# Optimization experiments

Hardware: AMD Instinct MI355X
Metric: run time of the kernel (lower is better)

Reference implementation:

```python
import jax, jax.numpy as jnp
import numpy as np

N_ROOMS = 128
N = 2 + N_ROOMS          # 2 external wall nodes + room nodes
T = 131072               # number of evaluation times
DT = 30.0                # seconds between evaluations
Q_LIM = 500.0
K_SCALE = 1e-5           # physical scaling of sigmoid(params) -> conductances [1/s]
DAY = 86400.0
TOUT_N = 1100            # hourly outside-temperature table covering the horizon


def setup_inputs() -> dict:
    key = jax.random.key(0)
    k1, k2, k3, k4 = jax.random.split(key, 4)
    t_eval = jnp.arange(T, dtype=jnp.float32) * DT
    params = jax.random.uniform(k1, (N * N,), dtype=jnp.float32)      # torch.rand init
    heating = jax.random.normal(k2, (N_ROOMS, 3), dtype=jnp.float32)  # torch.randn init
    B = jnp.zeros((N, 1 + N_ROOMS), dtype=jnp.float32)
    B = B.at[:, 0].set(jax.random.uniform(k3, (N,), dtype=jnp.float32) * 1e-5)  # Tout coupling
    B = B.at[2:, 1:].set(jnp.eye(N_ROOMS, dtype=jnp.float32) * 1e-6)           # heat input per room
    tout_t = jnp.arange(TOUT_N, dtype=jnp.float32) * 3600.0
    tout_v = 10.0 + 5.0 * jax.random.normal(k4, (TOUT_N,), dtype=jnp.float32)
    return {"t_eval": t_eval, "params": params, "heating": heating, "B": B,
            "tout_t": tout_t, "tout_v": tout_v}


def _forward(t_eval, params, heating, B, tout_t, tout_v):
    # transform + physical scaling of parameters -> RC conductance matrix A
    theta = jax.nn.sigmoid(params) * K_SCALE
    K = theta.reshape(N, N)
    d = jnp.diag(K)
    Koff = K - jnp.diag(d)
    A = Koff - jnp.diag(Koff.sum(axis=1) + d)   # Metzler, nonpositive row sums -> stable

    # transform + heat scaling -> continuous heating profile Qrms_continuous
    Q_avg = jax.nn.sigmoid(heating[:, 0]) * Q_LIM
    phase = heating[:, 1]
    sharp = heating[:, 2]

    t0 = t_eval[0]
    te = t_eval - t0
    two_pi = 2.0 * jnp.pi

    def Tout(t):  # Tout_continuous (linear interp, like scipy interp1d)
        return jnp.interp(t + t0, tout_t, tout_v)

    def Qf(t):    # smooth periodic heating schedule per room
        return Q_avg * jax.nn.sigmoid(sharp * jnp.sin(two_pi * (t + t0) / DAY + phase))

    def f(t, x):  # dx/dt = A @ x + B @ u
        u = jnp.concatenate([Tout(t)[None], Qf(t)])[:, None]   # [1+R, 1]
        return A @ x + B @ u

    iv = (Tout(te[0]) + 4.0) * jnp.ones((N, 1), dtype=jnp.float32)

    def step(x, tt):  # one RK4 step between consecutive evaluation times
        t, dt = tt
        half = dt * 0.5
        k1 = f(t, x)
        k2 = f(t + half, x + half * k1)
        k3 = f(t + half, x + half * k2)
        k4 = f(t + dt, x + dt * k3)
        xn = x + (dt / 6.0) * (k1 + 2.0 * k2 + 2.0 * k3 + k4)
        return xn, xn

    ts = te[:-1]
    dts = te[1:] - te[:-1]
    _, xs = jax.lax.scan(step, iv, (ts, dts))
    sol = jnp.concatenate([iv[None], xs], axis=0)   # [T, N, 1]
    return sol[:, 2:]                               # room temperatures only


def reference(t_eval, params, heating, B, tout_t, tout_v):
    return _forward(t_eval, params, heating, B, tout_t, tout_v)
```

## Files before the change

### kernel.cpp

```cpp
#include <hip/hip_runtime.h>
#include <math.h>

#define NPAD 132
#define TSTEPS 131071
#define LCH 128
#define NCH 1024
#define PERIOD 2880
#define OMEGA 7.2722052166430399e-05f

#define OFF_A    0
#define OFF_A2   17160
#define OFF_A3   34320
#define OFF_M    51480
#define OFF_C1   68640
#define OFF_C2   85800
#define OFF_P1   102960
#define OFF_P2   120120
#define OFF_M64  137280
#define OFF_M128 154440
#define OFF_M2K  171600
#define OFF_C1T  188760
#define OFF_C2T  205144
#define OFF_C1B  221528
#define OFF_C2B  221658
#define OFF_C3B  221788
#define OFF_AMP  221918
#define OFF_CPH  222046
#define OFF_SPH  222174
#define OFF_SH   222302
#define OFF_G    222430
#define OFF_S64  355550
#define OFF_XB   488670
#define OFF_XB2  621790
#define OFF_SA   888030
#define OFF_GP   896350
#define OFF_TT   1270750

__device__ __forceinline__ float sigm(float x) { return 1.0f / (1.0f + expf(-x)); }

__device__ __forceinline__ float interp_tout(float t, const float* __restrict__ tv) {
    float u = t * (1.0f / 3600.0f);
    int idx = (int)u;
    if (idx > 1098) idx = 1098;
    float fr = u - (float)idx;
    float v0 = tv[idx];
    return v0 + fr * (tv[idx + 1] - v0);
}

__global__ __launch_bounds__(256) void build_A_kernel(
    const float* __restrict__ params, const float* __restrict__ heating,
    const float* __restrict__ Bm, const float* __restrict__ tout_v,
    float* __restrict__ ws, float* __restrict__ out) {
    const int tid = threadIdx.x;
    float* A = ws + OFF_A;

    for (int idx = tid; idx < 130 * 130; idx += 256) {
        int r = idx / 130, c = idx - r * 130;
        A[r * NPAD + c] = sigm(params[idx]) * 1e-5f;
    }
    for (int r = tid; r < 130; r += 256) { A[r * NPAD + 130] = 0.f; A[r * NPAD + 131] = 0.f; }
    __syncthreads();
    for (int r = tid; r < 130; r += 256) {
        float s = 0.0f;
        for (int k = 0; k < 130; ++k) s += A[r * NPAD + k];
        A[r * NPAD + r] = -s;
    }
    for (int i = tid; i < 128; i += 256) {
        float bd = Bm[(2 + i) * 129 + (1 + i)];
        ws[OFF_AMP + i] = sigm(heating[i * 3]) * 500.0f * bd;
        float ph = heating[i * 3 + 1];
        ws[OFF_CPH + i] = cosf(ph);
        ws[OFF_SPH + i] = sinf(ph);
        ws[OFF_SH + i]  = heating[i * 3 + 2];
    }
    float iv = tout_v[0] + 4.0f;
    for (int i = tid; i < 128; i += 256) out[i] = iv;
    for (int r = tid; r < 130; r += 256) ws[OFF_XB + r] = iv;
}

__global__ __launch_bounds__(192) void mm_kernel(float* __restrict__ ws,
                                                 int offD, int offX, int offY) {
    const float* X = ws + offX;
    const float* Y = ws + offY;
    float* dst = ws + offD;
    __shared__ float xrow[130];
    const int r = blockIdx.x;
    const int c = threadIdx.x;
    if (c < 130) xrow[c] = X[r * NPAD + c];
    __syncthreads();
    if (c < 130) {
        float acc = 0.0f;
#pragma unroll 10
        for (int k = 0; k < 130; ++k)
            acc = fmaf(xrow[k], Y[k * NPAD + c], acc);
        dst[r * NPAD + c] = acc;
    }
    if (c >= 130 && c < 132) dst[r * NPAD + c] = 0.0f;
}

__global__ __launch_bounds__(192) void mm34_kernel(float* __restrict__ ws) {
    const int b = blockIdx.x;
    const bool hi = (b >= 130);
    const int r = hi ? b - 130 : b;
    const float* X = ws + (hi ? OFF_A2 : OFF_A);
    const float* Y = ws + OFF_A2;
    float* dst = ws + (hi ? OFF_P2 : OFF_A3);
    __shared__ float xrow[130];
    const int c = threadIdx.x;
    if (c < 130) xrow[c] = X[r * NPAD + c];
    __syncthreads();
    if (c < 130) {
        float acc = 0.0f;
#pragma unroll 10
        for (int k = 0; k < 130; ++k)
            acc = fmaf(xrow[k], Y[k * NPAD + c], acc);
        dst[r * NPAD + c] = acc;
    }
    if (c >= 130 && c < 132) dst[r * NPAD + c] = 0.0f;
}

__global__ __launch_bounds__(256) void combine_kernel(float* __restrict__ ws) {
    int idx = blockIdx.x * 256 + threadIdx.x;
    if (idx >= 130 * 130) return;
    int r = idx / 130, c = idx - r * 130;
    int o = r * NPAD + c;
    const float* A  = ws + OFF_A;
    const float* A2 = ws + OFF_A2;
    const float* A3 = ws + OFF_A3;
    const float* A4 = ws + OFF_P2;
    float eye = (r == c) ? 1.0f : 0.0f;
    float a = A[o], a2 = A2[o], a3 = A3[o], a4 = A4[o];
    float c1v = 5.0f * eye + 150.0f * a + 2250.0f * a2 + 33750.0f * a3;
    float c2v = 20.0f * eye + 300.0f * a + 2250.0f * a2;
    ws[OFF_M  + o] = eye + 30.0f * a + 450.0f * a2 + 4500.0f * a3 + 33750.0f * a4;
    ws[OFF_C1 + o] = c1v;
    ws[OFF_C2 + o] = c2v;
    if (r >= 2 && c >= 2) {
        ws[OFF_C1T + (c - 2) * 128 + (r - 2)] = c1v;
        ws[OFF_C2T + (c - 2) * 128 + (r - 2)] = c2v;
    }
    if (c == 0) {
        ws[OFF_M + r * NPAD + 130] = 0.f; ws[OFF_M + r * NPAD + 131] = 0.f;
        ws[OFF_C1 + r * NPAD + 130] = 0.f; ws[OFF_C1 + r * NPAD + 131] = 0.f;
        ws[OFF_C2 + r * NPAD + 130] = 0.f; ws[OFF_C2 + r * NPAD + 131] = 0.f;
    }
}

__global__ __launch_bounds__(192) void vecs_kernel(const float* __restrict__ Bm,
                                                   float* __restrict__ ws) {
    const int r = threadIdx.x;
    if (r >= 130) return;
    const float* C1 = ws + OFF_C1;
    const float* C2 = ws + OFF_C2;
    float s1 = 0.0f, s2 = 0.0f;
    for (int k = 0; k < 130; ++k) {
        float b0 = Bm[k * 129];
        s1 = fmaf(C1[r * NPAD + k], b0, s1);
        s2 = fmaf(C2[r * NPAD + k], b0, s2);
    }
    ws[OFF_C1B + r] = s1;
    ws[OFF_C2B + r] = s2;
    ws[OFF_C3B + r] = 5.0f * Bm[r * 129];
}

__global__ __launch_bounds__(256) void gper_kernel(float* __restrict__ ws) {
    const int tid = threadIdx.x;
    const int n0 = blockIdx.x * 32;
    const float* C1T = ws + OFF_C1T;
    const float* C2T = ws + OFF_C2T;
    const float* C1 = ws + OFF_C1;
    const float* C2 = ws + OFF_C2;
    const float* amp = ws + OFF_AMP;
    const float* cph = ws + OFF_CPH;
    const float* sph = ws + OFF_SPH;
    const float* sh  = ws + OFF_SH;
    float* P = ws + OFF_GP;

    __shared__ __align__(16) float qgT[128][36];
    __shared__ __align__(16) float qmT[128][36];
    __shared__ float sth[65], cth[65];

    for (int j = tid; j < 65; j += 256) {
        float t = (j < 33) ? (float)(n0 + j) * 30.0f
                           : (float)(n0 + j - 33) * 30.0f + 15.0f;
        float a = t * OMEGA;
        sth[j] = sinf(a);
        cth[j] = cosf(a);
    }
    __syncthreads();

    for (int p = tid; p < 65 * 128; p += 256) {
        int j = p >> 7, i = p & 127;
        float s = sth[j] * cph[i] + cth[j] * sph[i];
        float v = amp[i] / (1.0f + __expf(-sh[i] * s));
        if (j < 33) qgT[i][j] = v; else qmT[i][j - 33] = v;
    }
    __syncthreads();

    const int rr = tid & 127;
    const int half = tid >> 7;
    const int r = rr + 2;
    float acc1[16], acc2[16];
#pragma unroll
    for (int w = 0; w < 16; ++w) { acc1[w] = 0.0f; acc2[w] = 0.0f; }

    for (int k = 0; k < 128; ++k) {
        float c1 = C1T[(k << 7) + rr];
        float c2 = C2T[(k << 7) + rr];
        const float4* q1p = reinterpret_cast<const float4*>(&qgT[k][half * 16]);
        const float4* q2p = reinterpret_cast<const float4*>(&qmT[k][half * 16]);
#pragma unroll
        for (int w = 0; w < 4; ++w) {
            float4 a = q1p[w];
            float4 b = q2p[w];
            acc1[4 * w + 0] = fmaf(c1, a.x, acc1[4 * w + 0]);
            acc1[4 * w + 1] = fmaf(c1, a.y, acc1[4 * w + 1]);
            acc1[4 * w + 2] = fmaf(c1, a.z, acc1[4 * w + 2]);
            acc1[4 * w + 3] = fmaf(c1, a.w, acc1[4 * w + 3]);
            acc2[4 * w + 0] = fmaf(c2, b.x, acc2[4 * w + 0]);
            acc2[4 * w + 1] = fmaf(c2, b.y, acc2[4 * w + 1]);
            acc2[4 * w + 2] = fmaf(c2, b.z, acc2[4 * w + 2]);
            acc2[4 * w + 3] = fmaf(c2, b.w, acc2[4 * w + 3]);
        }
    }
#pragma unroll
    for (int w = 0; w < 16; ++w) {
        int n = half * 16 + w;
        P[(n0 + n) * 130 + r] = acc1[w] + acc2[w] + 5.0f * qgT[rr][n + 1];
    }

    if (tid < 64) {
        int r2 = tid >> 5;
        int n = tid & 31;
        float acc = 0.0f;
        for (int k = 0; k < 128; ++k) {
            acc = fmaf(C1[r2 * NPAD + 2 + k], qgT[k][n], acc);
            acc = fmaf(C2[r2 * NPAD + 2 + k], qmT[k][n], acc);
        }
        P[(n0 + n) * 130 + r2] = acc;
    }
}

__global__ __launch_bounds__(256) void ttab_kernel(const float* __restrict__ tout_v,
                                                   float* __restrict__ ws) {
    int n = blockIdx.x * 256 + threadIdx.x;
    if (n < 131072) {
        float t = (float)n * 30.0f;
        float2* TT = reinterpret_cast<float2*>(ws + OFF_TT);
        TT[n] = make_float2(interp_tout(t, tout_v), interp_tout(t + 15.0f, tout_v));
    }
}

__global__ __launch_bounds__(192, 3) void chunk_accum_kernel(float* __restrict__ ws) {
    const int c = blockIdx.x;
    const int r = threadIdx.x;
    const float* Mm = ws + OFF_M;
    const float* P = ws + OFF_GP;
    const float2* TT = reinterpret_cast<const float2*>(ws + OFF_TT);

    __shared__ __align__(16) float xs[2][132];
    float4 mr[33];
    float c1br = 0.f, c2br = 0.f, c3br = 0.f;
    if (r < 130) {
#pragma unroll
        for (int q = 0; q < 33; ++q)
            mr[q] = reinterpret_cast<const float4*>(&Mm[r * NPAD])[q];
        c1br = ws[OFF_C1B + r]; c2br = ws[OFF_C2B + r]; c3br = ws[OFF_C3B + r];
    }
    if (r < 132) { xs[0][r] = 0.0f; xs[1][r] = 0.0f; }
    __syncthreads();

    const int base = c * LCH;
    const int len = min(LCH, TSTEPS - base);
    int m = base % PERIOD;
    float pv = (r < 130) ? P[m * 130 + r] : 0.0f;
    float2 tc = TT[base], tn = TT[base + 1];
    int cur = 0;
    for (int j = 0; j < len; ++j) {
        if (r < 130) {
            float gcur = pv + tc.x * c1br + tc.y * c2br + tn.x * c3br;
            m = (m + 1 == PERIOD) ? 0 : m + 1;
            if (j + 1 < len) { pv = P[m * 130 + r]; tc = tn; tn = TT[base + j + 2]; }
            const float4* xp = reinterpret_cast<const float4*>(xs[cur]);
            float a0 = 0.f, a1 = 0.f, a2 = 0.f, a3 = 0.f;
#pragma unroll
            for (int q = 0; q < 33; ++q) {
                float4 xv = xp[q];
                a0 = fmaf(mr[q].x, xv.x, a0);
                a1 = fmaf(mr[q].y, xv.y, a1);
                a2 = fmaf(mr[q].z, xv.z, a2);
                a3 = fmaf(mr[q].w, xv.w, a3);
            }
            float val = (a0 + a1) + (a2 + a3) + gcur;
            xs[cur ^ 1][r] = val;
            if (j == 63) ws[OFF_S64 + c * 130 + r] = val;
        }
        __syncthreads();
        cur ^= 1;
    }
    if (r < 130) ws[OFF_G + c * 130 + r] = xs[cur][r];
}

__global__ __launch_bounds__(192, 3) void superaccum_kernel(float* __restrict__ ws) {
    const int s = blockIdx.x;
    const int r = threadIdx.x;
    const float* MP = ws + OFF_M128;
    const float* G = ws + OFF_G;

    __shared__ __align__(16) float xs[2][132];
    float4 mr[33];
    if (r < 130) {
#pragma unroll
        for (int q = 0; q < 33; ++q)
            mr[q] = reinterpret_cast<const float4*>(&MP[r * NPAD])[q];
    }
    if (r < 132) { xs[0][r] = 0.0f; xs[1][r] = 0.0f; }
    __syncthreads();

    int cur = 0;
    for (int i = 0; i < 16; ++i) {
        if (r < 130) {
            const float4* xp = reinterpret_cast<const float4*>(xs[cur]);
            float a0 = 0.f, a1 = 0.f, a2 = 0.f, a3 = 0.f;
#pragma unroll
            for (int q = 0; q < 33; ++q) {
                float4 xv = xp[q];
                a0 = fmaf(mr[q].x, xv.x, a0);
                a1 = fmaf(mr[q].y, xv.y, a1);
                a2 = fmaf(mr[q].z, xv.z, a2);
                a3 = fmaf(mr[q].w, xv.w, a3);
            }
            xs[cur ^ 1][r] = (a0 + a1) + (a2 + a3) + G[(16 * s + i) * 130 + r];
        }
        __syncthreads();
        cur ^= 1;
    }
    if (r < 130) ws[OFF_SA + s * 130 + r] = xs[cur][r];
}

__global__ __launch_bounds__(192, 3) void superbound_kernel(float* __restrict__ ws) {
    const int r = threadIdx.x;
    const float* M2K = ws + OFF_M2K;
    const float* SA = ws + OFF_SA;
    float* xb = ws + OFF_XB;

    __shared__ __align__(16) float xs[2][132];
    float4 mr[33];
    if (r < 130) {
#pragma unroll
        for (int q = 0; q < 33; ++q)
            mr[q] = reinterpret_cast<const float4*>(&M2K[r * NPAD])[q];
    }
    if (r < 132) { xs[0][r] = (r < 130) ? xb[r] : 0.0f; xs[1][r] = 0.0f; }
    __syncthreads();

    int cur = 0;
    for (int s = 0; s < 63; ++s) {
        if (r < 130) {
            const float4* xp = reinterpret_cast<const float4*>(xs[cur]);
            float a0 = 0.f, a1 = 0.f, a2 = 0.f, a3 = 0.f;
#pragma unroll
            for (int q = 0; q < 33; ++q) {
                float4 xv = xp[q];
                a0 = fmaf(mr[q].x, xv.x, a0);
                a1 = fmaf(mr[q].y, xv.y, a1);
                a2 = fmaf(mr[q].z, xv.z, a2);
                a3 = fmaf(mr[q].w, xv.w, a3);
            }
            float val = (a0 + a1) + (a2 + a3) + SA[s * 130 + r];
            xs[cur ^ 1][r] = val;
            xb[(16 * s + 16) * 130 + r] = val;
        }
        __syncthreads();
        cur ^= 1;
    }
}

__global__ __launch_bounds__(192, 3) void chunkbound_kernel(float* __restrict__ ws) {
    const int s = blockIdx.x;
    const int r = threadIdx.x;
    const float* MP = ws + OFF_M128;
    const float* G = ws + OFF_G;
    float* xb = ws + OFF_XB;

    __shared__ __align__(16) float xs[2][132];
    float4 mr[33];
    if (r < 130) {
#pragma unroll
        for (int q = 0; q < 33; ++q)
            mr[q] = reinterpret_cast<const float4*>(&MP[r * NPAD])[q];
    }
    if (r < 132) { xs[0][r] = (r < 130) ? xb[(16 * s) * 130 + r] : 0.0f; xs[1][r] = 0.0f; }
    __syncthreads();

    int cur = 0;
    for (int i = 0; i < 15; ++i) {
        if (r < 130) {
            const float4* xp = reinterpret_cast<const float4*>(xs[cur]);
            float a0 = 0.f, a1 = 0.f, a2 = 0.f, a3 = 0.f;
#pragma unroll
            for (int q = 0; q < 33; ++q) {
                float4 xv = xp[q];
                a0 = fmaf(mr[q].x, xv.x, a0);
                a1 = fmaf(mr[q].y, xv.y, a1);
                a2 = fmaf(mr[q].z, xv.z, a2);
                a3 = fmaf(mr[q].w, xv.w, a3);
            }
            float val = (a0 + a1) + (a2 + a3) + G[(16 * s + i) * 130 + r];
            xs[cur ^ 1][r] = val;
            xb[(16 * s + i + 1) * 130 + r] = val;
        }
        __syncthreads();
        cur ^= 1;
    }
}

__global__ __launch_bounds__(192, 3) void subbound_kernel(float* __restrict__ ws) {
    const int c = blockIdx.x;
    const int r = threadIdx.x;
    const float* M64 = ws + OFF_M64;
    const float* xb = ws + OFF_XB;
    float* xb2 = ws + OFF_XB2;

    __shared__ __align__(16) float xs[132];
    if (r < 132) xs[r] = (r < 130) ? xb[c * 130 + r] : 0.0f;
    __syncthreads();
    if (r < 130) {
        const float4* xp = reinterpret_cast<const float4*>(xs);
        const float4* mp = reinterpret_cast<const float4*>(&M64[r * NPAD]);
        float a0 = 0.f, a1 = 0.f, a2 = 0.f, a3 = 0.f;
#pragma unroll
        for (int q = 0; q < 33; ++q) {
            float4 m = mp[q];
            float4 xv = xp[q];
            a0 = fmaf(m.x, xv.x, a0);
            a1 = fmaf(m.y, xv.y, a1);
            a2 = fmaf(m.z, xv.z, a2);
            a3 = fmaf(m.w, xv.w, a3);
        }
        xb2[(2 * c) * 130 + r] = xs[r];
        xb2[(2 * c + 1) * 130 + r] = (a0 + a1) + (a2 + a3) + ws[OFF_S64 + c * 130 + r];
    }
}

__global__ __launch_bounds__(192, 3) void chunk_emit_kernel(float* __restrict__ ws,
                                                            float* __restrict__ out) {
    const int ec = blockIdx.x;
    const int r = threadIdx.x;
    const float* Mm = ws + OFF_M;
    const float* P = ws + OFF_GP;
    const float2* TT = reinterpret_cast<const float2*>(ws + OFF_TT);
    const float* xb2 = ws + OFF_XB2;

    __shared__ __align__(16) float xs[2][132];
    float4 mr[33];
    float c1br = 0.f, c2br = 0.f, c3br = 0.f;
    if (r < 130) {
#pragma unroll
        for (int q = 0; q < 33; ++q)
            mr[q] = reinterpret_cast<const float4*>(&Mm[r * NPAD])[q];
        c1br = ws[OFF_C1B + r]; c2br = ws[OFF_C2B + r]; c3br = ws[OFF_C3B + r];
    }
    if (r < 132) { xs[0][r] = (r < 130) ? xb2[ec * 130 + r] : 0.0f; xs[1][r] = 0.0f; }
    __syncthreads();

    const int base = ec * 64;
    const int len = min(64, TSTEPS - base);
    int m = base % PERIOD;
    float pv = (r < 130) ? P[m * 130 + r] : 0.0f;
    float2 tc = TT[base], tn = TT[base + 1];
    int cur = 0;
    for (int j = 0; j < len; ++j) {
        if (r < 130) {
            float gcur = pv + tc.x * c1br + tc.y * c2br + tn.x * c3br;
            m = (m + 1 == PERIOD) ? 0 : m + 1;
            if (j + 1 < len) { pv = P[m * 130 + r]; tc = tn; tn = TT[base + j + 2]; }
            const float4* xp = reinterpret_cast<const float4*>(xs[cur]);
            float a0 = 0.f, a1 = 0.f, a2 = 0.f, a3 = 0.f;
#pragma unroll
            for (int q = 0; q < 33; ++q) {
                float4 xv = xp[q];
                a0 = fmaf(mr[q].x, xv.x, a0);
                a1 = fmaf(mr[q].y, xv.y, a1);
                a2 = fmaf(mr[q].z, xv.z, a2);
                a3 = fmaf(mr[q].w, xv.w, a3);
            }
            float val = (a0 + a1) + (a2 + a3) + gcur;
            xs[cur ^ 1][r] = val;
            if (r >= 2) out[(base + j + 1) * 128 + (r - 2)] = val;
        }
        __syncthreads();
        cur ^= 1;
    }
}

extern "C" void kernel_launch(void* const* d_in, const int* in_sizes, int n_in,
                              void* d_out, int out_size, void* d_ws, size_t ws_size,
                              hipStream_t stream) {
    const float* params  = (const float*)d_in[1];
    const float* heating = (const float*)d_in[2];
    const float* Bm      = (const float*)d_in[3];
    const float* tout_v  = (const float*)d_in[5];
    float* out = (float*)d_out;
    float* ws = (float*)d_ws;

    build_A_kernel<<<1, 256, 0, stream>>>(params, heating, Bm, tout_v, ws, out);

    mm_kernel<<<130, 192, 0, stream>>>(ws, OFF_A2, OFF_A, OFF_A);
    mm34_kernel<<<260, 192, 0, stream>>>(ws);
    combine_kernel<<<67, 256, 0, stream>>>(ws);
    vecs_kernel<<<1, 192, 0, stream>>>(Bm, ws);
    gper_kernel<<<90, 256, 0, stream>>>(ws);
    ttab_kernel<<<512, 256, 0, stream>>>(tout_v, ws);

    mm_kernel<<<130, 192, 0, stream>>>(ws, OFF_P1,   OFF_M,    OFF_M);
    mm_kernel<<<130, 192, 0, stream>>>(ws, OFF_P2,   OFF_P1,   OFF_P1);
    mm_kernel<<<130, 192, 0, stream>>>(ws, OFF_P1,   OFF_P2,   OFF_P2);
    mm_kernel<<<130, 192, 0, stream>>>(ws, OFF_P2,   OFF_P1,   OFF_P1);
    mm_kernel<<<130, 192, 0, stream>>>(ws, OFF_P1,   OFF_P2,   OFF_P2);
    mm_kernel<<<130, 192, 0, stream>>>(ws, OFF_M64,  OFF_P1,   OFF_P1);
    mm_kernel<<<130, 192, 0, stream>>>(ws, OFF_M128, OFF_M64,  OFF_M64);
    mm_kernel<<<130, 192, 0, stream>>>(ws, OFF_P1,   OFF_M128, OFF_M128);
    mm_kernel<<<130, 192, 0, stream>>>(ws, OFF_P2,   OFF_P1,   OFF_P1);
    mm_kernel<<<130, 192, 0, stream>>>(ws, OFF_P1,   OFF_P2,   OFF_P2);
    mm_kernel<<<130, 192, 0, stream>>>(ws, OFF_M2K,  OFF_P1,   OFF_P1);

    chunk_accum_kernel<<<NCH, 192, 0, stream>>>(ws);
    superaccum_kernel<<<63, 192, 0, stream>>>(ws);
    superbound_kernel<<<1, 192, 0, stream>>>(ws);
    chunkbound_kernel<<<64, 192, 0, stream>>>(ws);
    subbound_kernel<<<NCH, 192, 0, stream>>>(ws);
    chunk_emit_kernel<<<2 * NCH, 192, 0, stream>>>(ws, out);
}
```

Measured before the change: 537.1 us.

## Stride-4 chunk accumulation using M^4 and precomputed 4-step forcing tables

The chunk accumulation pass now advances four RK4 steps per matrix-vector product using M^4. It uses a doubled periodic forcing table (GP4, built by two new pdouble kernels) and nine per-row weights for the outside-temperature samples, precomputed in vecs2. This cuts the serial matvec-and-barrier count in the accumulation phase by a factor of four, at the cost of extra setup kernels and more workspace. Launch bounds drop from 3 to 2 blocks per CU, and inline asm pins keep the matrix rows in registers. This may reduce occupancy and changes rounding order.

```diff
diff --git a/kernel.cpp b/kernel.cpp
--- a/kernel.cpp
+++ b/kernel.cpp
@@ -16,25 +16,32 @@
 #define OFF_C2   85800
 #define OFF_P1   102960
 #define OFF_P2   120120
-#define OFF_M64  137280
-#define OFF_M128 154440
-#define OFF_M2K  171600
-#define OFF_C1T  188760
-#define OFF_C2T  205144
-#define OFF_C1B  221528
-#define OFF_C2B  221658
-#define OFF_C3B  221788
-#define OFF_AMP  221918
-#define OFF_CPH  222046
-#define OFF_SPH  222174
-#define OFF_SH   222302
-#define OFF_G    222430
-#define OFF_S64  355550
-#define OFF_XB   488670
-#define OFF_XB2  621790
-#define OFF_SA   888030
-#define OFF_GP   896350
-#define OFF_TT   1270750
+#define OFF_M2   137280
+#define OFF_M4   154440
+#define OFF_M64  171600
+#define OFF_M128 188760
+#define OFF_M2K  205920
+#define OFF_C1T  223080
+#define OFF_C2T  239464
+#define OFF_C1B  255848
+#define OFF_C2B  255978
+#define OFF_C3B  256108
+#define OFF_AMP  256238
+#define OFF_CPH  256366
+#define OFF_SPH  256494
+#define OFF_SH   256622
+#define OFF_W    256750
+#define OFF_G    257920
+#define OFF_S64  391040
+#define OFF_XB   524160
+#define OFF_XB2  657280
+#define OFF_SA   923520
+#define OFF_GP   931710
+#define OFF_GP2  1306110
+#define OFF_GP4  1680510
+#define OFF_TT   2054910
+
+#define PIN4(v) asm volatile("" : "+v"((v).x), "+v"((v).y), "+v"((v).z), "+v"((v).w))
 
 __device__ __forceinline__ float sigm(float x) { return 1.0f / (1.0f + expf(-x)); }
 
@@ -146,21 +153,59 @@
     }
 }
 
-__global__ __launch_bounds__(192) void vecs_kernel(const float* __restrict__ Bm,
-                                                   float* __restrict__ ws) {
+__global__ __launch_bounds__(192) void vecs2_kernel(const float* __restrict__ Bm,
+                                                    float* __restrict__ ws) {
     const int r = threadIdx.x;
-    if (r >= 130) return;
     const float* C1 = ws + OFF_C1;
     const float* C2 = ws + OFF_C2;
-    float s1 = 0.0f, s2 = 0.0f;
-    for (int k = 0; k < 130; ++k) {
-        float b0 = Bm[k * 129];
-        s1 = fmaf(C1[r * NPAD + k], b0, s1);
-        s2 = fmaf(C2[r * NPAD + k], b0, s2);
-    }
-    ws[OFF_C1B + r] = s1;
-    ws[OFF_C2B + r] = s2;
-    ws[OFF_C3B + r] = 5.0f * Bm[r * 129];
+    const float* Mm = ws + OFF_M;
+    __shared__ __align__(16) float va[132], vb[132], vd[132];
+    __shared__ __align__(16) float na[132], nb[132], nd[132];
+    __shared__ float a1s[130], a2s[130], c1bs[130];
+
+    if (r < 132) { va[r] = 0.f; vb[r] = 0.f; vd[r] = 0.f; na[r] = 0.f; nb[r] = 0.f; nd[r] = 0.f; }
+    __syncthreads();
+    if (r < 130) {
+        float s1 = 0.0f, s2 = 0.0f;
+        for (int k = 0; k < 130; ++k) {
+            float b0 = Bm[k * 129];
+            s1 = fmaf(C1[r * NPAD + k], b0, s1);
+            s2 = fmaf(C2[r * NPAD + k], b0, s2);
+        }
+        float c3 = 5.0f * Bm[r * 129];
+        ws[OFF_C1B + r] = s1; ws[OFF_C2B + r] = s2; ws[OFF_C3B + r] = c3;
+        ws[OFF_W + 7 * 130 + r] = s2;
+        ws[OFF_W + 8 * 130 + r] = c3;
+        va[r] = s1; vb[r] = s2; vd[r] = c3; c1bs[r] = s1;
+    }
+    __syncthreads();
+
+    for (int st = 1; st <= 3; ++st) {
+        if (r < 130) {
+            const float4* mp = reinterpret_cast<const float4*>(&Mm[r * NPAD]);
+            const float4* pa = reinterpret_cast<const float4*>(va);
+            const float4* pb = reinterpret_cast<const float4*>(vb);
+            const float4* pd = reinterpret_cast<const float4*>(vd);
+            float aa = 0.f, ab = 0.f, ad = 0.f;
+#pragma unroll
+            for (int q = 0; q < 33; ++q) {
+                float4 m = mp[q];
+                float4 xa = pa[q], xb = pb[q], xd = pd[q];
+                aa = fmaf(m.x, xa.x, fmaf(m.y, xa.y, fmaf(m.z, xa.z, fmaf(m.w, xa.w, aa))));
+                ab = fmaf(m.x, xb.x, fmaf(m.y, xb.y, fmaf(m.z, xb.z, fmaf(m.w, xb.w, ab))));
+                ad = fmaf(m.x, xd.x, fmaf(m.y, xd.y, fmaf(m.z, xd.z, fmaf(m.w, xd.w, ad))));
+            }
+            na[r] = aa; nb[r] = ab; nd[r] = ad;
+        }
+        __syncthreads();
+        if (r < 130) {
+            if (st == 1) { ws[OFF_W + 5 * 130 + r] = nb[r]; ws[OFF_W + 6 * 130 + r] = nd[r] + c1bs[r]; a1s[r] = na[r]; }
+            if (st == 2) { ws[OFF_W + 3 * 130 + r] = nb[r]; ws[OFF_W + 4 * 130 + r] = nd[r] + a1s[r]; a2s[r] = na[r]; }
+            if (st == 3) { ws[OFF_W + 0 * 130 + r] = na[r]; ws[OFF_W + 1 * 130 + r] = nb[r]; ws[OFF_W + 2 * 130 + r] = nd[r] + a2s[r]; }
+            va[r] = na[r]; vb[r] = nb[r]; vd[r] = nd[r];
+        }
+        __syncthreads();
+    }
 }
 
 __global__ __launch_bounds__(256) void gper_kernel(float* __restrict__ ws) {
@@ -241,46 +286,88 @@
     }
 }
 
+__global__ __launch_bounds__(192) void pdouble_kernel(float* __restrict__ ws,
+                                                      int offD, int offS, int offMat, int shift) {
+    const int m0 = blockIdx.x * 16;
+    const int tid = threadIdx.x;
+    const float* S = ws + offS;
+    const float* Mat = ws + offMat;
+    float* D = ws + offD;
+    __shared__ __align__(16) float xs2[16][132];
+    for (int p = tid; p < 16 * 132; p += 192) {
+        int i = p / 132, rr = p - i * 132;
+        xs2[i][rr] = (rr < 130) ? S[(m0 + i) * 130 + rr] : 0.0f;
+    }
+    __syncthreads();
+    const int r = tid;
+    if (r < 130) {
+        float acc[16];
+#pragma unroll
+        for (int i = 0; i < 16; ++i) acc[i] = 0.0f;
+        const float4* mp = reinterpret_cast<const float4*>(&Mat[r * NPAD]);
+        for (int q = 0; q < 33; ++q) {
+            float4 m = mp[q];
+#pragma unroll
+            for (int i = 0; i < 16; ++i) {
+                float4 x = reinterpret_cast<const float4*>(xs2[i])[q];
+                acc[i] = fmaf(m.x, x.x, fmaf(m.y, x.y, fmaf(m.z, x.z, fmaf(m.w, x.w, acc[i]))));
+            }
+        }
+#pragma unroll
+        for (int i = 0; i < 16; ++i) {
+            int ms = m0 + i + shift; if (ms >= PERIOD) ms -= PERIOD;
+            D[(m0 + i) * 130 + r] = acc[i] + S[ms * 130 + r];
+        }
+    }
+}
+
 __global__ __launch_bounds__(256) void ttab_kernel(const float* __restrict__ tout_v,
                                                    float* __restrict__ ws) {
     int n = blockIdx.x * 256 + threadIdx.x;
-    if (n < 131072) {
+    if (n < 131080) {
         float t = (float)n * 30.0f;
         float2* TT = reinterpret_cast<float2*>(ws + OFF_TT);
         TT[n] = make_float2(interp_tout(t, tout_v), interp_tout(t + 15.0f, tout_v));
     }
 }
 
-__global__ __launch_bounds__(192, 3) void chunk_accum_kernel(float* __restrict__ ws) {
+__global__ __launch_bounds__(192, 2) void chunk_accum_kernel(float* __restrict__ ws) {
     const int c = blockIdx.x;
     const int r = threadIdx.x;
-    const float* Mm = ws + OFF_M;
-    const float* P = ws + OFF_GP;
+    const float* M4 = ws + OFF_M4;
+    const float* P4 = ws + OFF_GP4;
     const float2* TT = reinterpret_cast<const float2*>(ws + OFF_TT);
 
     __shared__ __align__(16) float xs[2][132];
     float4 mr[33];
-    float c1br = 0.f, c2br = 0.f, c3br = 0.f;
-    if (r < 130) {
-#pragma unroll
-        for (int q = 0; q < 33; ++q)
-            mr[q] = reinterpret_cast<const float4*>(&Mm[r * NPAD])[q];
-        c1br = ws[OFF_C1B + r]; c2br = ws[OFF_C2B + r]; c3br = ws[OFF_C3B + r];
+    float w0 = 0.f, w1 = 0.f, w2 = 0.f, w3 = 0.f, w4 = 0.f, w5 = 0.f, w6 = 0.f, w7 = 0.f, w8 = 0.f;
+    if (r < 130) {
+#pragma unroll
+        for (int q = 0; q < 33; ++q) {
+            mr[q] = reinterpret_cast<const float4*>(&M4[r * NPAD])[q];
+            PIN4(mr[q]);
+        }
+        w0 = ws[OFF_W + 0 * 130 + r]; w1 = ws[OFF_W + 1 * 130 + r]; w2 = ws[OFF_W + 2 * 130 + r];
+        w3 = ws[OFF_W + 3 * 130 + r]; w4 = ws[OFF_W + 4 * 130 + r]; w5 = ws[OFF_W + 5 * 130 + r];
+        w6 = ws[OFF_W + 6 * 130 + r]; w7 = ws[OFF_W + 7 * 130 + r]; w8 = ws[OFF_W + 8 * 130 + r];
     }
     if (r < 132) { xs[0][r] = 0.0f; xs[1][r] = 0.0f; }
     __syncthreads();
 
     const int base = c * LCH;
-    const int len = min(LCH, TSTEPS - base);
-    int m = base % PERIOD;
-    float pv = (r < 130) ? P[m * 130 + r] : 0.0f;
-    float2 tc = TT[base], tn = TT[base + 1];
+    int mu = base % PERIOD;
+    float pv = (r < 130) ? P4[mu * 130 + r] : 0.0f;
     int cur = 0;
-    for (int j = 0; j < len; ++j) {
+    for (int u = 0; u < 32; ++u) {
         if (r < 130) {
-            float gcur = pv + tc.x * c1br + tc.y * c2br + tn.x * c3br;
-            m = (m + 1 == PERIOD) ? 0 : m + 1;
-            if (j + 1 < len) { pv = P[m * 130 + r]; tc = tn; tn = TT[base + j + 2]; }
+            const int n = base + 4 * u;
+            float2 t0 = TT[n], t1 = TT[n + 1], t2 = TT[n + 2], t3 = TT[n + 3];
+            float tg4 = TT[n + 4].x;
+            float gcur = pv
+                + t0.x * w0 + t0.y * w1 + t1.x * w2 + t1.y * w3
+                + t2.x * w4 + t2.y * w5 + t3.x * w6 + t3.y * w7 + tg4 * w8;
+            mu = (mu + 4 >= PERIOD) ? mu + 4 - PERIOD : mu + 4;
+            if (u + 1 < 32) pv = P4[mu * 130 + r];
             const float4* xp = reinterpret_cast<const float4*>(xs[cur]);
             float a0 = 0.f, a1 = 0.f, a2 = 0.f, a3 = 0.f;
 #pragma unroll
@@ -293,7 +380,7 @@
             }
             float val = (a0 + a1) + (a2 + a3) + gcur;
             xs[cur ^ 1][r] = val;
-            if (j == 63) ws[OFF_S64 + c * 130 + r] = val;
+            if (u == 15) ws[OFF_S64 + c * 130 + r] = val;
         }
         __syncthreads();
         cur ^= 1;
@@ -301,7 +388,7 @@
     if (r < 130) ws[OFF_G + c * 130 + r] = xs[cur][r];
 }
 
-__global__ __launch_bounds__(192, 3) void superaccum_kernel(float* __restrict__ ws) {
+__global__ __launch_bounds__(192, 2) void superaccum_kernel(float* __restrict__ ws) {
     const int s = blockIdx.x;
     const int r = threadIdx.x;
     const float* MP = ws + OFF_M128;
@@ -311,8 +398,10 @@
     float4 mr[33];
     if (r < 130) {
 #pragma unroll
-        for (int q = 0; q < 33; ++q)
+        for (int q = 0; q < 33; ++q) {
             mr[q] = reinterpret_cast<const float4*>(&MP[r * NPAD])[q];
+            PIN4(mr[q]);
+        }
     }
     if (r < 132) { xs[0][r] = 0.0f; xs[1][r] = 0.0f; }
     __syncthreads();
@@ -338,7 +427,7 @@
     if (r < 130) ws[OFF_SA + s * 130 + r] = xs[cur][r];
 }
 
-__global__ __launch_bounds__(192, 3) void superbound_kernel(float* __restrict__ ws) {
+__global__ __launch_bounds__(192, 2) void superbound_kernel(float* __restrict__ ws) {
     const int r = threadIdx.x;
     const float* M2K = ws + OFF_M2K;
     const float* SA = ws + OFF_SA;
@@ -348,8 +437,10 @@
     float4 mr[33];
     if (r < 130) {
 #pragma unroll
-        for (int q = 0; q < 33; ++q)
+        for (int q = 0; q < 33; ++q) {
             mr[q] = reinterpret_cast<const float4*>(&M2K[r * NPAD])[q];
+            PIN4(mr[q]);
+        }
     }
     if (r < 132) { xs[0][r] = (r < 130) ? xb[r] : 0.0f; xs[1][r] = 0.0f; }
     __syncthreads();
@@ -376,7 +467,7 @@
     }
 }
 
-__global__ __launch_bounds__(192, 3) void chunkbound_kernel(float* __restrict__ ws) {
+__global__ __launch_bounds__(192, 2) void chunkbound_kernel(float* __restrict__ ws) {
     const int s = blockIdx.x;
     const int r = threadIdx.x;
     const float* MP = ws + OFF_M128;
@@ -387,8 +478,10 @@
     float4 mr[33];
     if (r < 130) {
 #pragma unroll
-        for (int q = 0; q < 33; ++q)
+        for (int q = 0; q < 33; ++q) {
             mr[q] = reinterpret_cast<const float4*>(&MP[r * NPAD])[q];
+            PIN4(mr[q]);
+        }
     }
     if (r < 132) { xs[0][r] = (r < 130) ? xb[(16 * s) * 130 + r] : 0.0f; xs[1][r] = 0.0f; }
     __syncthreads();
@@ -415,7 +508,7 @@
     }
 }
 
-__global__ __launch_bounds__(192, 3) void subbound_kernel(float* __restrict__ ws) {
+__global__ __launch_bounds__(192, 2) void subbound_kernel(float* __restrict__ ws) {
     const int c = blockIdx.x;
     const int r = threadIdx.x;
     const float* M64 = ws + OFF_M64;
@@ -443,7 +536,7 @@
     }
 }
 
-__global__ __launch_bounds__(192, 3) void chunk_emit_kernel(float* __restrict__ ws,
+__global__ __launch_bounds__(192, 2) void chunk_emit_kernel(float* __restrict__ ws,
                                                             float* __restrict__ out) {
     const int ec = blockIdx.x;
     const int r = threadIdx.x;
@@ -457,8 +550,10 @@
     float c1br = 0.f, c2br = 0.f, c3br = 0.f;
     if (r < 130) {
 #pragma unroll
-        for (int q = 0; q < 33; ++q)
+        for (int q = 0; q < 33; ++q) {
             mr[q] = reinterpret_cast<const float4*>(&Mm[r * NPAD])[q];
+            PIN4(mr[q]);
+        }
         c1br = ws[OFF_C1B + r]; c2br = ws[OFF_C2B + r]; c3br = ws[OFF_C3B + r];
     }
     if (r < 132) { xs[0][r] = (r < 130) ? xb2[ec * 130 + r] : 0.0f; xs[1][r] = 0.0f; }
@@ -509,13 +604,13 @@
     mm_kernel<<<130, 192, 0, stream>>>(ws, OFF_A2, OFF_A, OFF_A);
     mm34_kernel<<<260, 192, 0, stream>>>(ws);
     combine_kernel<<<67, 256, 0, stream>>>(ws);
-    vecs_kernel<<<1, 192, 0, stream>>>(Bm, ws);
+    vecs2_kernel<<<1, 192, 0, stream>>>(Bm, ws);
     gper_kernel<<<90, 256, 0, stream>>>(ws);
-    ttab_kernel<<<512, 256, 0, stream>>>(tout_v, ws);
-
-    mm_kernel<<<130, 192, 0, stream>>>(ws, OFF_P1,   OFF_M,    OFF_M);
-    mm_kernel<<<130, 192, 0, stream>>>(ws, OFF_P2,   OFF_P1,   OFF_P1);
-    mm_kernel<<<130, 192, 0, stream>>>(ws, OFF_P1,   OFF_P2,   OFF_P2);
+    ttab_kernel<<<513, 256, 0, stream>>>(tout_v, ws);
+
+    mm_kernel<<<130, 192, 0, stream>>>(ws, OFF_M2,   OFF_M,    OFF_M);
+    mm_kernel<<<130, 192, 0, stream>>>(ws, OFF_M4,   OFF_M2,   OFF_M2);
+    mm_kernel<<<130, 192, 0, stream>>>(ws, OFF_P1,   OFF_M4,   OFF_M4);
     mm_kernel<<<130, 192, 0, stream>>>(ws, OFF_P2,   OFF_P1,   OFF_P1);
     mm_kernel<<<130, 192, 0, stream>>>(ws, OFF_P1,   OFF_P2,   OFF_P2);
     mm_kernel<<<130, 192, 0, stream>>>(ws, OFF_M64,  OFF_P1,   OFF_P1);
@@ -525,6 +620,9 @@
     mm_kernel<<<130, 192, 0, stream>>>(ws, OFF_P1,   OFF_P2,   OFF_P2);
     mm_kernel<<<130, 192, 0, stream>>>(ws, OFF_M2K,  OFF_P1,   OFF_P1);
 
+    pdouble_kernel<<<180, 192, 0, stream>>>(ws, OFF_GP2, OFF_GP,  OFF_M,  1);
+    pdouble_kernel<<<180, 192, 0, stream>>>(ws, OFF_GP4, OFF_GP2, OFF_M2, 2);
+
     chunk_accum_kernel<<<NCH, 192, 0, stream>>>(ws);
     superaccum_kernel<<<63, 192, 0, stream>>>(ws);
     superbound_kernel<<<1, 192, 0, stream>>>(ws);
```

New measurement: 588.3 us. 9.5% more time.
